# Optimization experiments

Hardware: AMD Instinct MI355X
Metric: run time of the kernel (lower is better)

Reference implementation:

```python
import jax, jax.numpy as jnp
import numpy as np
from jax.scipy.special import logsumexp

B, S, L = 1024, 8192, 3


def setup_inputs() -> dict:
    key = jax.random.key(0)
    k1, k2, k3, k4, k5 = jax.random.split(key, 5)
    emissions = jax.random.normal(k1, (B, S, L), dtype=jnp.float32)
    labels = jax.random.randint(k2, (B, S), 0, L, dtype=jnp.int64)
    start_transitions = 0.1 * jax.random.normal(k3, (L,), dtype=jnp.float32)
    transitions = 0.1 * jax.random.normal(k4, (L, L), dtype=jnp.float32)
    end_transitions = 0.1 * jax.random.normal(k5, (L,), dtype=jnp.float32)
    return {
        "emissions": emissions,
        "labels": labels,
        "start_transitions": start_transitions,
        "transitions": transitions,
        "end_transitions": end_transitions,
    }


def reference(emissions, labels, start_transitions, transitions, end_transitions):
    # mask is all-ones in the original module, so every timestep is valid.
    # --- log partition via forward algorithm (sequential DP over time) ---
    alpha0 = start_transitions[None, :] + emissions[:, 0]  # [B, L]

    def step(alpha, e_t):
        # alpha: [B, L] (prev label), e_t: [B, L] (next label)
        nxt = logsumexp(alpha[:, :, None] + transitions[None, :, :] + e_t[:, None, :], axis=1)
        return nxt, None

    e_rest = jnp.swapaxes(emissions[:, 1:], 0, 1)  # [S-1, B, L]
    alphaT, _ = jax.lax.scan(step, alpha0, e_rest)
    log_z = logsumexp(alphaT + end_transitions[None, :], axis=-1)  # [B]

    # --- gold path score ---
    em_score = jnp.take_along_axis(emissions, labels[:, :, None], axis=2)[..., 0].sum(axis=1)  # [B]
    trans_score = transitions[labels[:, :-1], labels[:, 1:]].sum(axis=1)  # [B]
    score = start_transitions[labels[:, 0]] + em_score + trans_score + end_transitions[labels[:, -1]]

    log_likelihood = jnp.sum(score - log_z)  # torchcrf default reduction='sum'
    return -log_likelihood
```

## Files before the change

kernel.cpp:

```cpp
#include <hip/hip_runtime.h>

typedef float f32x2 __attribute__((ext_vector_type(2)));

#define LOG2E 1.44269504088896340736f
#define LN2   0.69314718055994530942f
#define S_    8192
#define WSTEP 1024
#define NCH   8
#define NWAVE 4

#if __has_builtin(__builtin_amdgcn_exp2f)
__device__ __forceinline__ float exp2f_(float x){ return __builtin_amdgcn_exp2f(x); }
#else
__device__ __forceinline__ float exp2f_(float x){ return __expf(x * LN2); }
#endif
#if __has_builtin(__builtin_amdgcn_logf)
__device__ __forceinline__ float log2f_(float x){ return __builtin_amdgcn_logf(x); }
#else
__device__ __forceinline__ float log2f_(float x){ return __logf(x) * LOG2E; }
#endif

#define RNORM(L0,L1,L2,H0,H1,H2,S2) { \
    f32x2 _m2 = __builtin_elementwise_max(__builtin_elementwise_max(L0,L1),L2); \
    float _m  = fmaxf(fmaxf(_m2.x,_m2.y), fmaxf(fmaxf(H0,H1),H2)); \
    int _e = (__float_as_int(_m) >> 23) & 0xff; \
    float _rs = __int_as_float((254 - _e) << 23); \
    L0*=_rs; L1*=_rs; L2*=_rs; H0*=_rs; H1*=_rs; H2*=_rs; \
    S2 += (float)(_e - 127); }

#define STEPM(L0,L1,L2,H0,H1,H2, ea,eb,ec) { \
    float _E0=__expf(ea), _E1=__expf(eb), _E2=__expf(ec); \
    f32x2 _n0=(L0*W00+L1*W10+L2*W20)*_E0; float _q0=(H0*W00+H1*W10+H2*W20)*_E0; \
    f32x2 _n1=(L0*W01+L1*W11+L2*W21)*_E1; float _q1=(H0*W01+H1*W11+H2*W21)*_E1; \
    f32x2 _n2=(L0*W02+L1*W12+L2*W22)*_E2; float _q2=(H0*W02+H1*W12+H2*W22)*_E2; \
    L0=_n0; L1=_n1; L2=_n2; H0=_q0; H1=_q1; H2=_q2; }

#define COMBINE(AL0,AL1,AL2,AH0,AH1,AH2, BL0,BL1,BL2,BH0,BH1,BH2) { \
    f32x2 _c0 = AL0*BL0.x + AL1*BL0.y + AL2*BH0; \
    float _d0 = AH0*BL0.x + AH1*BL0.y + AH2*BH0; \
    f32x2 _c1 = AL0*BL1.x + AL1*BL1.y + AL2*BH1; \
    float _d1 = AH0*BL1.x + AH1*BL1.y + AH2*BH1; \
    f32x2 _c2 = AL0*BL2.x + AL1*BL2.y + AL2*BH2; \
    float _d2 = AH0*BL2.x + AH1*BL2.y + AH2*BH2; \
    AL0=_c0; AL1=_c1; AL2=_c2; AH0=_d0; AH1=_d1; AH2=_d2; }

__device__ __forceinline__ void mul33(float* C, const float* A, const float* B){
#pragma unroll
    for (int i=0;i<3;i++){
        float a0=A[i*3], a1=A[i*3+1], a2=A[i*3+2];
#pragma unroll
        for (int j=0;j<3;j++)
            C[i*3+j] = a0*B[j] + a1*B[3+j] + a2*B[6+j];
    }
}
__device__ __forceinline__ void renorm9(float* V, float& s){
    float m = fmaxf(fmaxf(fmaxf(V[0],V[1]),fmaxf(V[2],V[3])),
                    fmaxf(fmaxf(V[4],V[5]),fmaxf(V[6],V[7])));
    m = fmaxf(m, V[8]);
    int e = (__float_as_int(m) >> 23) & 0xff;
    float rs = __int_as_float((254 - e) << 23);
#pragma unroll
    for (int k=0;k<9;++k) V[k] *= rs;
    s += (float)(e - 127);
}

extern "C" __global__ __launch_bounds__(256)
void crf_fwd(const float* __restrict__ em, const int* __restrict__ lab,
             const float* __restrict__ stt, const float* __restrict__ trt,
             const float* __restrict__ ent, float* __restrict__ ws)
{
    const int wv = threadIdx.x >> 6, ln = threadIdx.x & 63;
    const int g = blockIdx.x*NWAVE + wv;
    const int b = g >> 3, h = g & 7;

    __shared__ float tTw[NWAVE][12];
    if (ln < 9) tTw[wv][ln] = trt[ln];

    const float* emB = em + ((size_t)b*S_ + (size_t)h*WSTEP)*3;
    const int*   lbB = lab + (size_t)b*S_ + h*WSTEP;

    float ew[48];
    {
        const float4* ep = (const float4*)emB + ln*12;
#pragma unroll
        for (int k=0;k<12;++k){
            float4 v = ep[k];
            ew[4*k]=v.x; ew[4*k+1]=v.y; ew[4*k+2]=v.z; ew[4*k+3]=v.w;
        }
    }
    int pa, pb, lastl;
    {
        const int4* lp = (const int4*)lbB + ln*4;
        int4 a = lp[0], c = lp[1], d = lp[2], e = lp[3];
        pa = a.x | (a.y<<2) | (a.z<<4) | (a.w<<6) | (c.x<<8) | (c.y<<10) | (c.z<<12) | (c.w<<14);
        pb = d.x | (d.y<<2) | (d.z<<4) | (d.w<<6) | (e.x<<8) | (e.y<<10) | (e.z<<12) | (e.w<<14);
        lastl = e.w;
    }

    float W00=__expf(trt[0]), W01=__expf(trt[1]), W02=__expf(trt[2]);
    float W10=__expf(trt[3]), W11=__expf(trt[4]), W12=__expf(trt[5]);
    float W20=__expf(trt[6]), W21=__expf(trt[7]), W22=__expf(trt[8]);
    float st0=stt[0], st1=stt[1], st2=stt[2];

    int prevA = __shfl_up(lastl, 1, 64);
    if (ln == 0) prevA = (h == 0) ? 0 : lbB[-1];
    int prevB = (pa >> 14) & 3;
    const bool head = (h==0 && ln==0);

    f32x2 AL0={1,0}, AL1={0,1}, AL2={0,0};  float AH0=0, AH1=0, AH2=1;
    f32x2 BL0={1,0}, BL1={0,1}, BL2={0,0};  float BH0=0, BH1=0, BH2=1;
    float S2 = 0.f, sc = 0.f;

#pragma unroll
    for (int s=0; s<8; ++s){
        {
            float ea=ew[3*s], eb=ew[3*s+1], ec=ew[3*s+2];
            int l = (pa >> (2*s)) & 3;
            float ee = (l==1) ? eb : ((l==2) ? ec : ea);
            if (head && s==0){
                float sv = (l==1) ? st1 : ((l==2) ? st2 : st0);
                sc += sv + ee;
            } else {
                sc += tTw[wv][prevA*3+l] + ee;
            }
            prevA = l;
            if (!(head && s==0)) STEPM(AL0,AL1,AL2,AH0,AH1,AH2, ea,eb,ec);
        }
        {
            float ea=ew[24+3*s], eb=ew[24+3*s+1], ec=ew[24+3*s+2];
            int l = (pb >> (2*s)) & 3;
            float ee = (l==1) ? eb : ((l==2) ? ec : ea);
            sc += tTw[wv][prevB*3+l] + ee;
            prevB = l;
            STEPM(BL0,BL1,BL2,BH0,BH1,BH2, ea,eb,ec);
        }
        if (s==3 || s==7){
            RNORM(AL0,AL1,AL2,AH0,AH1,AH2, S2);
            RNORM(BL0,BL1,BL2,BH0,BH1,BH2, S2);
        }
    }

    COMBINE(AL0,AL1,AL2,AH0,AH1,AH2, BL0,BL1,BL2,BH0,BH1,BH2);
    RNORM(AL0,AL1,AL2,AH0,AH1,AH2, S2);

#pragma unroll
    for (int off=1; off<64; off<<=1){
        f32x2 bL0, bL1, bL2; float bH0, bH1, bH2, bS2;
        bL0.x=__shfl_down(AL0.x,(unsigned)off,64); bL0.y=__shfl_down(AL0.y,(unsigned)off,64);
        bL1.x=__shfl_down(AL1.x,(unsigned)off,64); bL1.y=__shfl_down(AL1.y,(unsigned)off,64);
        bL2.x=__shfl_down(AL2.x,(unsigned)off,64); bL2.y=__shfl_down(AL2.y,(unsigned)off,64);
        bH0=__shfl_down(AH0,(unsigned)off,64); bH1=__shfl_down(AH1,(unsigned)off,64);
        bH2=__shfl_down(AH2,(unsigned)off,64); bS2=__shfl_down(S2,(unsigned)off,64);
        COMBINE(AL0,AL1,AL2,AH0,AH1,AH2, bL0,bL1,bL2,bH0,bH1,bH2);
        S2 += bS2;
        RNORM(AL0,AL1,AL2,AH0,AH1,AH2, S2);
    }
#pragma unroll
    for (int off=32; off; off>>=1) sc += __shfl_down(sc, (unsigned)off, 64);

    if (ln == 0){
        float4* r = (float4*)(ws + (size_t)g*16);
        r[0] = make_float4(AL0.x, AL1.x, AL2.x, AL0.y);
        r[1] = make_float4(AL1.y, AL2.y, AH0,   AH1);
        r[2] = make_float4(AH2,   S2,    sc,    ew[0]);
        r[3] = make_float4(ew[1], ew[2], 0.f,   0.f);
    }
}

extern "C" __global__ __launch_bounds__(64)
void crf_fin1(const float* __restrict__ ws, const float* __restrict__ stt,
              const float* __restrict__ ent, float* __restrict__ partial)
{
    const int q = blockIdx.x*64 + threadIdx.x;
    const float* rr = ws + (size_t)q*NCH*16;
    float C[9], S = rr[9], sc = rr[10];
#pragma unroll
    for (int k=0;k<9;++k) C[k]=rr[k];
#pragma unroll
    for (int p=1;p<NCH;++p){
        const float* r = rr + p*16;
        float T[9]; mul33(T, C, r);
        S += r[9]; sc += r[10];
        renorm9(T, S);
#pragma unroll
        for (int k=0;k<9;++k) C[k]=T[k];
    }
    float a0=(stt[0]+rr[11])*LOG2E, a1=(stt[1]+rr[12])*LOG2E, a2=(stt[2]+rr[13])*LOG2E;
    float am = fmaxf(fmaxf(a0,a1),a2);
    float w0=exp2f_(a0-am), w1=exp2f_(a1-am), w2=exp2f_(a2-am);
    float q0=w0*C[0]+w1*C[3]+w2*C[6];
    float q1=w0*C[1]+w1*C[4]+w2*C[7];
    float q2=w0*C[2]+w1*C[5]+w2*C[8];
    float z = q0*exp2f_(ent[0]*LOG2E) + q1*exp2f_(ent[1]*LOG2E) + q2*exp2f_(ent[2]*LOG2E);
    float logz = (am + S + log2f_(z)) * LN2;
    float nll = logz - sc;
#pragma unroll
    for (int off=32; off; off>>=1) nll += __shfl_down(nll, (unsigned)off, 64);
    if (threadIdx.x==0) partial[blockIdx.x] = nll;
}

extern "C" __global__ __launch_bounds__(64)
void crf_fin2(const float* __restrict__ partial, float* __restrict__ out)
{
    float v = (threadIdx.x < 16) ? partial[threadIdx.x] : 0.f;
#pragma unroll
    for (int off=32; off; off>>=1) v += __shfl_down(v, (unsigned)off, 64);
    if (threadIdx.x==0) out[0] = v;
}

extern "C" void kernel_launch(void* const* d_in, const int* in_sizes, int n_in,
                              void* d_out, int out_size, void* d_ws, size_t ws_size,
                              hipStream_t stream) {
    const float* em  = (const float*)d_in[0];
    const int*   lab = (const int*)d_in[1];
    const float* stt = (const float*)d_in[2];
    const float* trt = (const float*)d_in[3];
    const float* ent = (const float*)d_in[4];
    float* out = (float*)d_out;
    float* ws  = (float*)d_ws;
    const int B = in_sizes[1] / S_;
    float* partial = ws + (size_t)NCH*B*16;

    crf_fwd<<<B*NCH/NWAVE, 256, 0, stream>>>(em, lab, stt, trt, ent, ws);
    crf_fin1<<<B/64, 64, 0, stream>>>(ws, stt, ent, partial);
    crf_fin2<<<1, 64, 0, stream>>>(partial, out);
}
```

Before: 184.6 us.

## Halve per-wave chunk and stage emissions via direct global-to-LDS loads

Each wave now covers 512 timesteps instead of 1024, doubling the wave count to 16 chunks per sequence. Emissions are staged into swizzled shared memory with global_load_lds 16-byte transfers, then read back per lane. Labels are kept as plain ints instead of packed 2-bit fields, and the transition table moves from shared memory to registers. The goal is more parallelism and coalesced loads with fewer registers per lane. The cost is that fin1 must combine twice as many chunk matrices, and the code depends on the global_load_lds builtin being available.

Measured after the change: 187.2 us. No clear change (+1.4%).

```diff
diff --git a/kernel.cpp b/kernel.cpp
--- a/kernel.cpp
+++ b/kernel.cpp
@@ -5,8 +5,9 @@
 #define LOG2E 1.44269504088896340736f
 #define LN2   0.69314718055994530942f
 #define S_    8192
-#define WSTEP 1024
-#define NCH   8
+#define WSTEP 512
+#define NCH   16
+#define TPB   256
 #define NWAVE 4
 
 #if __has_builtin(__builtin_amdgcn_exp2f)
@@ -20,6 +21,13 @@
 __device__ __forceinline__ float log2f_(float x){ return __logf(x) * LOG2E; }
 #endif
 
+__device__ __forceinline__ void gload16(const void* g, void* l){
+#if __has_builtin(__builtin_amdgcn_global_load_lds)
+    __builtin_amdgcn_global_load_lds((const __attribute__((address_space(1))) void*)g,
+                                     (__attribute__((address_space(3))) void*)l, 16, 0, 0);
+#endif
+}
+
 #define RNORM(L0,L1,L2,H0,H1,H2,S2) { \
     f32x2 _m2 = __builtin_elementwise_max(__builtin_elementwise_max(L0,L1),L2); \
     float _m  = fmaxf(fmaxf(_m2.x,_m2.y), fmaxf(fmaxf(H0,H1),H2)); \
@@ -64,82 +72,90 @@
     s += (float)(e - 127);
 }
 
-extern "C" __global__ __launch_bounds__(256)
+extern "C" __global__ __launch_bounds__(TPB)
 void crf_fwd(const float* __restrict__ em, const int* __restrict__ lab,
              const float* __restrict__ stt, const float* __restrict__ trt,
              const float* __restrict__ ent, float* __restrict__ ws)
 {
     const int wv = threadIdx.x >> 6, ln = threadIdx.x & 63;
     const int g = blockIdx.x*NWAVE + wv;
-    const int b = g >> 3, h = g & 7;
-
-    __shared__ float tTw[NWAVE][12];
-    if (ln < 9) tTw[wv][ln] = trt[ln];
+    const int b = g >> 4, h = g & 15;
+
+    __shared__ float4 emS[NWAVE*384];
+    float4* myS = emS + wv*384;
 
     const float* emB = em + ((size_t)b*S_ + (size_t)h*WSTEP)*3;
     const int*   lbB = lab + (size_t)b*S_ + h*WSTEP;
 
-    float ew[48];
     {
-        const float4* ep = (const float4*)emB + ln*12;
-#pragma unroll
-        for (int k=0;k<12;++k){
-            float4 v = ep[k];
-            ew[4*k]=v.x; ew[4*k+1]=v.y; ew[4*k+2]=v.z; ew[4*k+3]=v.w;
-        }
-    }
-    int pa, pb, lastl;
-    {
-        const int4* lp = (const int4*)lbB + ln*4;
-        int4 a = lp[0], c = lp[1], d = lp[2], e = lp[3];
-        pa = a.x | (a.y<<2) | (a.z<<4) | (a.w<<6) | (c.x<<8) | (c.y<<10) | (c.z<<12) | (c.w<<14);
-        pb = d.x | (d.y<<2) | (d.z<<4) | (d.w<<6) | (e.x<<8) | (e.y<<10) | (e.z<<12) | (e.w<<14);
-        lastl = e.w;
-    }
+        const char* gb = (const char*)emB;
+        char* lb = (char*)myS;
+        const int ksw = ln ^ ((ln >> 3) & 7);
+#pragma unroll
+        for (int i=0;i<6;++i)
+            gload16(gb + (size_t)(i*64 + ksw)*16, lb + i*1024);
+    }
+
+    const int4* lb4 = (const int4*)lbB;
+    int4 lv0 = lb4[2*ln], lv1 = lb4[2*ln+1];
 
     float W00=__expf(trt[0]), W01=__expf(trt[1]), W02=__expf(trt[2]);
     float W10=__expf(trt[3]), W11=__expf(trt[4]), W12=__expf(trt[5]);
     float W20=__expf(trt[6]), W21=__expf(trt[7]), W22=__expf(trt[8]);
+    float tT[9] = {trt[0],trt[1],trt[2],trt[3],trt[4],trt[5],trt[6],trt[7],trt[8]};
     float st0=stt[0], st1=stt[1], st2=stt[2];
 
-    int prevA = __shfl_up(lastl, 1, 64);
+    const bool head = (h==0 && ln==0);
+    int prevA = __shfl_up(lv1.w, 1, 64);
     if (ln == 0) prevA = (h == 0) ? 0 : lbB[-1];
-    int prevB = (pa >> 14) & 3;
-    const bool head = (h==0 && ln==0);
+    int prevB = lv0.w;
+
+    asm volatile("s_waitcnt vmcnt(0)" ::: "memory");
+    __builtin_amdgcn_sched_barrier(0);
+
+    float ew[24];
+    {
+        const int v0 = 6*ln;
+#pragma unroll
+        for (int r=0;r<6;++r){
+            int v = v0 + r;
+            int u = v ^ ((v >> 3) & 7);
+            *(float4*)&ew[4*r] = myS[u];
+        }
+    }
 
     f32x2 AL0={1,0}, AL1={0,1}, AL2={0,0};  float AH0=0, AH1=0, AH2=1;
     f32x2 BL0={1,0}, BL1={0,1}, BL2={0,0};  float BH0=0, BH1=0, BH2=1;
     float S2 = 0.f, sc = 0.f;
-
-#pragma unroll
-    for (int s=0; s<8; ++s){
+    int la[4] = {lv0.x, lv0.y, lv0.z, lv0.w};
+    int lb_[4] = {lv1.x, lv1.y, lv1.z, lv1.w};
+
+#pragma unroll
+    for (int s=0; s<4; ++s){
         {
             float ea=ew[3*s], eb=ew[3*s+1], ec=ew[3*s+2];
-            int l = (pa >> (2*s)) & 3;
+            int l = la[s];
             float ee = (l==1) ? eb : ((l==2) ? ec : ea);
             if (head && s==0){
                 float sv = (l==1) ? st1 : ((l==2) ? st2 : st0);
                 sc += sv + ee;
             } else {
-                sc += tTw[wv][prevA*3+l] + ee;
+                sc += tT[prevA*3+l] + ee;
             }
             prevA = l;
             if (!(head && s==0)) STEPM(AL0,AL1,AL2,AH0,AH1,AH2, ea,eb,ec);
         }
         {
-            float ea=ew[24+3*s], eb=ew[24+3*s+1], ec=ew[24+3*s+2];
-            int l = (pb >> (2*s)) & 3;
+            float ea=ew[12+3*s], eb=ew[12+3*s+1], ec=ew[12+3*s+2];
+            int l = lb_[s];
             float ee = (l==1) ? eb : ((l==2) ? ec : ea);
-            sc += tTw[wv][prevB*3+l] + ee;
+            sc += tT[prevB*3+l] + ee;
             prevB = l;
             STEPM(BL0,BL1,BL2,BH0,BH1,BH2, ea,eb,ec);
         }
-        if (s==3 || s==7){
-            RNORM(AL0,AL1,AL2,AH0,AH1,AH2, S2);
-            RNORM(BL0,BL1,BL2,BH0,BH1,BH2, S2);
-        }
-    }
-
+    }
+    RNORM(AL0,AL1,AL2,AH0,AH1,AH2, S2);
+    RNORM(BL0,BL1,BL2,BH0,BH1,BH2, S2);
     COMBINE(AL0,AL1,AL2,AH0,AH1,AH2, BL0,BL1,BL2,BH0,BH1,BH2);
     RNORM(AL0,AL1,AL2,AH0,AH1,AH2, S2);
 
@@ -221,7 +237,7 @@
     const int B = in_sizes[1] / S_;
     float* partial = ws + (size_t)NCH*B*16;
 
-    crf_fwd<<<B*NCH/NWAVE, 256, 0, stream>>>(em, lab, stt, trt, ent, ws);
+    crf_fwd<<<B*NCH/NWAVE, TPB, 0, stream>>>(em, lab, stt, trt, ent, ws);
     crf_fin1<<<B/64, 64, 0, stream>>>(ws, stt, ent, partial);
     crf_fin2<<<1, 64, 0, stream>>>(partial, out);
 }
```
